# Performance work log

Hardware: AMD Instinct MI355X
Metric: run time of the kernel (lower is better)

## Reference

```python
import jax, jax.numpy as jnp
import numpy as np
import math

N, T, D, H = 64, 512, 256, 256

def setup_inputs() -> dict:
    key = jax.random.key(0)
    k1, k2, k3, k4 = jax.random.split(key, 4)
    x = jax.random.normal(k1, (N, T, D), dtype=jnp.float32)
    h0 = jax.random.normal(k2, (N, H), dtype=jnp.float32)
    Wx = jax.random.normal(k3, (D, H), dtype=jnp.float32) / math.sqrt(D)
    Wh = jax.random.normal(k4, (H, H), dtype=jnp.float32) / math.sqrt(H)
    b = jnp.zeros((H,), dtype=jnp.float32)
    return {"x": x, "h0": h0, "Wx": Wx, "Wh": Wh, "b": b}

def reference(x, h0, Wx, Wh, b):
    # Precompute input projection for all timesteps in one big GEMM: (N,T,H)
    xW = jnp.einsum("ntd,dh->nth", x, Wx) + b
    def step(prev_h, xWt):
        next_h = jnp.tanh(xWt + prev_h @ Wh)
        return next_h, next_h
    # scan over time axis; xW transposed to (T,N,H)
    _, hs = jax.lax.scan(step, h0, jnp.swapaxes(xW, 0, 1))
    return jnp.swapaxes(hs, 0, 1)  # (N,T,H)
```

## Files before the change

### kernel.cpp

```cpp
#include <hip/hip_runtime.h>
#include <hip/hip_bf16.h>
#include <cmath>


#define KDIM  256
#define HDIM  256
#define TSTEPS 512
#define NBATCH 64
#define SCAN_BLOCKS 64
#define CH_STEPS 64
#define NCH 8
#define GEMM_BLOCKS (NCH * NBATCH)
#define SMEM_BYTES 41984

__device__ __forceinline__ unsigned pack2(float lo, float hi) {
    _Float16 fa = (_Float16)lo, fb = (_Float16)hi;
    unsigned short a, b;
    __builtin_memcpy(&a, &fa, 2);
    __builtin_memcpy(&b, &fb, 2);
    return (unsigned)a | ((unsigned)b << 16);
}

#define FMAMIX16(ACC, P0,P1,P2,P3,P4,P5,P6,P7)                                 \
    asm("v_fma_mix_f32 %0, %1, %17, %0 op_sel:[0,0,0] op_sel_hi:[0,1,0]\n\t"   \
        "v_fma_mix_f32 %0, %2, %17, %0 op_sel:[0,1,0] op_sel_hi:[0,1,0]\n\t"   \
        "v_fma_mix_f32 %0, %3, %18, %0 op_sel:[0,0,0] op_sel_hi:[0,1,0]\n\t"   \
        "v_fma_mix_f32 %0, %4, %18, %0 op_sel:[0,1,0] op_sel_hi:[0,1,0]\n\t"   \
        "v_fma_mix_f32 %0, %5, %19, %0 op_sel:[0,0,0] op_sel_hi:[0,1,0]\n\t"   \
        "v_fma_mix_f32 %0, %6, %19, %0 op_sel:[0,1,0] op_sel_hi:[0,1,0]\n\t"   \
        "v_fma_mix_f32 %0, %7, %20, %0 op_sel:[0,0,0] op_sel_hi:[0,1,0]\n\t"   \
        "v_fma_mix_f32 %0, %8, %20, %0 op_sel:[0,1,0] op_sel_hi:[0,1,0]\n\t"   \
        "v_fma_mix_f32 %0, %9, %21, %0 op_sel:[0,0,0] op_sel_hi:[0,1,0]\n\t"   \
        "v_fma_mix_f32 %0, %10, %21, %0 op_sel:[0,1,0] op_sel_hi:[0,1,0]\n\t"  \
        "v_fma_mix_f32 %0, %11, %22, %0 op_sel:[0,0,0] op_sel_hi:[0,1,0]\n\t"  \
        "v_fma_mix_f32 %0, %12, %22, %0 op_sel:[0,1,0] op_sel_hi:[0,1,0]\n\t"  \
        "v_fma_mix_f32 %0, %13, %23, %0 op_sel:[0,0,0] op_sel_hi:[0,1,0]\n\t"  \
        "v_fma_mix_f32 %0, %14, %23, %0 op_sel:[0,1,0] op_sel_hi:[0,1,0]\n\t"  \
        "v_fma_mix_f32 %0, %15, %24, %0 op_sel:[0,0,0] op_sel_hi:[0,1,0]\n\t"  \
        "v_fma_mix_f32 %0, %16, %24, %0 op_sel:[0,1,0] op_sel_hi:[0,1,0]\n\t"  \
        : "+v"(ACC)                                                            \
        : "v"(h0), "v"(h1), "v"(h2), "v"(h3),                                  \
          "v"(h4), "v"(h5), "v"(h6), "v"(h7),                                  \
          "v"(h8), "v"(h9), "v"(h10), "v"(h11),                                \
          "v"(h12), "v"(h13), "v"(h14), "v"(h15),                              \
          "v"(P0), "v"(P1), "v"(P2), "v"(P3),                                  \
          "v"(P4), "v"(P5), "v"(P6), "v"(P7))

#define LDW2(K)                                                                \
    float4 ta##K = *(const float4*)(wp + (2*(K)) * HDIM);                      \
    float4 tb##K = *(const float4*)(wp + (2*(K)+1) * HDIM);                    \
    unsigned wA##K = pack2(ta##K.x, tb##K.x);                                  \
    unsigned wB##K = pack2(ta##K.y, tb##K.y);                                  \
    unsigned wC##K = pack2(ta##K.z, tb##K.z);                                  \
    unsigned wD##K = pack2(ta##K.w, tb##K.w);

#define PIN8(P)                                                                \
    asm volatile("" : "+v"(P##0), "+v"(P##1), "+v"(P##2), "+v"(P##3),          \
                      "+v"(P##4), "+v"(P##5), "+v"(P##6), "+v"(P##7))

__global__ __launch_bounds__(1024) void fused(
    const float* __restrict__ x,
    const float* __restrict__ h0v,
    const float* __restrict__ Wx,
    const float* __restrict__ Wh,
    const float* __restrict__ bias,
    float* __restrict__ out,
    unsigned int* flags,
    int mode)
{
    __shared__ __align__(16) char smem[SMEM_BYTES];
    const int tid = threadIdx.x;

    if (mode == 1 && blockIdx.x < SCAN_BLOCKS) return;
    const bool is_scan = (mode == 2) || (mode == 0 && blockIdx.x < SCAN_BLOCKS);

    if (!is_scan) {
        float (*As)[68]  = (float(*)[68])smem;
        float (*Bs)[260] = (float(*)[260])(smem + 8704);

        const int bm = (int)blockIdx.x - SCAN_BLOCKS;
        const int r  = bm & 63;
        const int ch = bm >> 6;
        const int m0 = r * TSTEPS + ch * CH_STEPS;
        const int tx = tid & 63;
        const int ty = tid >> 6;

        float acc[4][4];
#pragma unroll
        for (int i = 0; i < 4; ++i)
#pragma unroll
            for (int j = 0; j < 4; ++j) acc[i][j] = 0.f;

        for (int kc = 0; kc < KDIM; kc += 32) {
            if (tid < 512) {
                int arow = tid >> 3;
                int ac4  = (tid & 7) << 2;
                float4 va = *(const float4*)&x[(size_t)(m0 + arow) * KDIM + kc + ac4];
                As[ac4 + 0][arow] = va.x;
                As[ac4 + 1][arow] = va.y;
                As[ac4 + 2][arow] = va.z;
                As[ac4 + 3][arow] = va.w;
            }
            {
                int brow = tid >> 6;
                int bc4  = (tid & 63) << 2;
                *(float4*)&Bs[brow][bc4] =
                    *(const float4*)&Wx[(size_t)(kc + brow) * HDIM + bc4];
                *(float4*)&Bs[brow + 16][bc4] =
                    *(const float4*)&Wx[(size_t)(kc + brow + 16) * HDIM + bc4];
            }
            __syncthreads();

#pragma unroll
            for (int kk = 0; kk < 32; ++kk) {
                float4 a = *(const float4*)&As[kk][ty * 4];
                float4 b = *(const float4*)&Bs[kk][tx * 4];
                acc[0][0] += a.x * b.x; acc[0][1] += a.x * b.y;
                acc[0][2] += a.x * b.z; acc[0][3] += a.x * b.w;
                acc[1][0] += a.y * b.x; acc[1][1] += a.y * b.y;
                acc[1][2] += a.y * b.z; acc[1][3] += a.y * b.w;
                acc[2][0] += a.z * b.x; acc[2][1] += a.z * b.y;
                acc[2][2] += a.z * b.z; acc[2][3] += a.z * b.w;
                acc[3][0] += a.w * b.x; acc[3][1] += a.w * b.y;
                acc[3][2] += a.w * b.z; acc[3][3] += a.w * b.w;
            }
            __syncthreads();
        }

        float4 bj = *(const float4*)&bias[tx * 4];
#pragma unroll
        for (int i = 0; i < 4; ++i) {
            float4 v;
            v.x = acc[i][0] + bj.x;
            v.y = acc[i][1] + bj.y;
            v.z = acc[i][2] + bj.z;
            v.w = acc[i][3] + bj.w;
            *(float4*)&out[(size_t)(m0 + ty * 4 + i) * HDIM + tx * 4] = v;
        }

        if (mode == 0) {
            __syncthreads();
            if (tid == 0)
                __hip_atomic_fetch_add(&flags[r * NCH + ch], 1u,
                                       __ATOMIC_RELEASE, __HIP_MEMORY_SCOPE_AGENT);
        }
        return;
    }

    float* h = (float*)smem;
    float (*red)[256] = (float(*)[256])(smem + 1024);

    const int r   = (int)blockIdx.x;
    const int jq  = tid & 63;
    const int g   = tid >> 6;
    const int j0  = jq << 2;

    const float* wp = Wh + (size_t)(g * 16) * HDIM + j0;
    LDW2(0) LDW2(1) LDW2(2) LDW2(3) LDW2(4) LDW2(5) LDW2(6) LDW2(7)
    PIN8(wA); PIN8(wB); PIN8(wC); PIN8(wD);

    if (tid < 256) h[tid] = h0v[(size_t)r * HDIM + tid];

    float* outr = out + (size_t)r * TSTEPS * HDIM;
    __syncthreads();

    float c_next = 0.f;
    for (int ch = 0; ch < NCH; ++ch) {
        if (mode == 0) {
            if (tid == 0) {
                const unsigned int* f = &flags[r * NCH + ch];
                while (__hip_atomic_load(f, __ATOMIC_RELAXED,
                                         __HIP_MEMORY_SCOPE_AGENT) == 0u)
                    __builtin_amdgcn_s_sleep(8);
                (void)__hip_atomic_load(f, __ATOMIC_ACQUIRE,
                                        __HIP_MEMORY_SCOPE_AGENT);
            }
            __syncthreads();
        }
        if (g < 4) c_next = outr[(size_t)(ch * CH_STEPS) * HDIM + tid];

        for (int tt = 0; tt < CH_STEPS; ++tt) {
            const int t = ch * CH_STEPS + tt;
            float c = c_next;
            if (g < 4 && tt + 1 < CH_STEPS)
                c_next = outr[(size_t)(t + 1) * HDIM + tid];

            const float4* hv = (const float4*)(h + (g << 4));
            float4 ha = hv[0], hb = hv[1], hc = hv[2], hd = hv[3];
            float h0 = ha.x, h1 = ha.y, h2 = ha.z, h3 = ha.w;
            float h4 = hb.x, h5 = hb.y, h6 = hb.z, h7 = hb.w;
            float h8 = hc.x, h9 = hc.y, h10 = hc.z, h11 = hc.w;
            float h12 = hd.x, h13 = hd.y, h14 = hd.z, h15 = hd.w;

            float a0 = 0.f, a1 = 0.f, a2 = 0.f, a3 = 0.f;
            FMAMIX16(a0, wA0,wA1,wA2,wA3,wA4,wA5,wA6,wA7);
            FMAMIX16(a1, wB0,wB1,wB2,wB3,wB4,wB5,wB6,wB7);
            FMAMIX16(a2, wC0,wC1,wC2,wC3,wC4,wC5,wC6,wC7);
            FMAMIX16(a3, wD0,wD1,wD2,wD3,wD4,wD5,wD6,wD7);

            float4 accv; accv.x = a0; accv.y = a1; accv.z = a2; accv.w = a3;
            *(float4*)&red[g][j0] = accv;
            __syncthreads();

            if (tid < 256) {
                float s0 = red[0][tid] + red[1][tid];
                float s1 = red[2][tid] + red[3][tid];
                float s2 = red[4][tid] + red[5][tid];
                float s3 = red[6][tid] + red[7][tid];
                float s4 = red[8][tid] + red[9][tid];
                float s5 = red[10][tid] + red[11][tid];
                float s6 = red[12][tid] + red[13][tid];
                float s7 = red[14][tid] + red[15][tid];
                float s  = (((s0 + s1) + (s2 + s3)) + ((s4 + s5) + (s6 + s7))) + c;
                float e  = __expf(2.f * s);
                float hn = 1.f - 2.f / (e + 1.f);
                outr[(size_t)t * HDIM + tid] = hn;
                h[tid] = hn;
            }
            __syncthreads();
        }
    }
}

extern "C" void kernel_launch(void* const* d_in, const int* in_sizes, int n_in,
                              void* d_out, int out_size, void* d_ws, size_t ws_size,
                              hipStream_t stream) {
    const float* x  = (const float*)d_in[0];
    const float* h0 = (const float*)d_in[1];
    const float* Wx = (const float*)d_in[2];
    const float* Wh = (const float*)d_in[3];
    const float* b  = (const float*)d_in[4];
    float* out = (float*)d_out;

    const size_t flag_bytes = (size_t)NBATCH * NCH * sizeof(unsigned int);
    if (d_ws != nullptr && ws_size >= flag_bytes) {
        unsigned int* flags = (unsigned int*)d_ws;
        hipMemsetAsync(d_ws, 0, flag_bytes, stream);
        fused<<<SCAN_BLOCKS + GEMM_BLOCKS, 1024, 0, stream>>>(
            x, h0, Wx, Wh, b, out, flags, 0);
    } else {
        fused<<<SCAN_BLOCKS + GEMM_BLOCKS, 1024, 0, stream>>>(
            x, h0, Wx, Wh, b, out, nullptr, 1);
        fused<<<SCAN_BLOCKS, 1024, 0, stream>>>(
            x, h0, Wx, Wh, b, out, nullptr, 2);
    }
}
```

Baseline: 534.3 us.

## Prepack Wh to fp16 globally and reload weights each step to free VGPRs

Adds a small pre-kernel that packs Wh into fp16 pairs in a global buffer laid out for the scan threads. The scan loop no longer keeps the 32 packed weight registers pinned. It reloads them from the (cache-resident) packed buffer every timestep, placed after the FMAs, with an opaque index so the loads are not hoisted. This cuts register pressure and setup conversion, at the cost of an extra launch and per-step global/L2 loads on the serial critical path.

```diff
diff --git a/kernel.cpp b/kernel.cpp
--- a/kernel.cpp
+++ b/kernel.cpp
@@ -13,12 +13,29 @@
 #define GEMM_BLOCKS (NCH * NBATCH)
 #define SMEM_BYTES 41984
 
+__device__ uint4 g_Wp[8192];
+
 __device__ __forceinline__ unsigned pack2(float lo, float hi) {
     _Float16 fa = (_Float16)lo, fb = (_Float16)hi;
     unsigned short a, b;
     __builtin_memcpy(&a, &fa, 2);
     __builtin_memcpy(&b, &fb, 2);
     return (unsigned)a | ((unsigned)b << 16);
+}
+
+__global__ __launch_bounds__(256) void pack_wh(const float* __restrict__ Wh) {
+    int idx = blockIdx.x * 256 + threadIdx.x;
+    int jq = idx & 63;
+    int gp = idx >> 6;
+    int g = gp >> 3, p = gp & 7;
+    const float* r0 = Wh + (size_t)(g * 16 + 2 * p) * HDIM + jq * 4;
+    const float* r1 = r0 + HDIM;
+    uint4 o;
+    o.x = pack2(r0[0], r1[0]);
+    o.y = pack2(r0[1], r1[1]);
+    o.z = pack2(r0[2], r1[2]);
+    o.w = pack2(r0[3], r1[3]);
+    g_Wp[idx] = o;
 }
 
 #define FMAMIX16(ACC, P0,P1,P2,P3,P4,P5,P6,P7)                                 \
@@ -46,23 +63,18 @@
           "v"(P0), "v"(P1), "v"(P2), "v"(P3),                                  \
           "v"(P4), "v"(P5), "v"(P6), "v"(P7))
 
-#define LDW2(K)                                                                \
-    float4 ta##K = *(const float4*)(wp + (2*(K)) * HDIM);                      \
-    float4 tb##K = *(const float4*)(wp + (2*(K)+1) * HDIM);                    \
-    unsigned wA##K = pack2(ta##K.x, tb##K.x);                                  \
-    unsigned wB##K = pack2(ta##K.y, tb##K.y);                                  \
-    unsigned wC##K = pack2(ta##K.z, tb##K.z);                                  \
-    unsigned wD##K = pack2(ta##K.w, tb##K.w);
-
-#define PIN8(P)                                                                \
-    asm volatile("" : "+v"(P##0), "+v"(P##1), "+v"(P##2), "+v"(P##3),          \
-                      "+v"(P##4), "+v"(P##5), "+v"(P##6), "+v"(P##7))
+#define LOADW do {                                                             \
+        unsigned _i = 0;                                                       \
+        asm volatile("" : "+v"(_i));                                           \
+        const uint4* wq = wbase + _i;                                          \
+        u0 = wq[0];   u1 = wq[64];  u2 = wq[128]; u3 = wq[192];                \
+        u4 = wq[256]; u5 = wq[320]; u6 = wq[384]; u7 = wq[448];                \
+    } while (0)
 
 __global__ __launch_bounds__(1024) void fused(
     const float* __restrict__ x,
     const float* __restrict__ h0v,
     const float* __restrict__ Wx,
-    const float* __restrict__ Wh,
     const float* __restrict__ bias,
     float* __restrict__ out,
     unsigned int* flags,
@@ -155,9 +167,9 @@
     const int g   = tid >> 6;
     const int j0  = jq << 2;
 
-    const float* wp = Wh + (size_t)(g * 16) * HDIM + j0;
-    LDW2(0) LDW2(1) LDW2(2) LDW2(3) LDW2(4) LDW2(5) LDW2(6) LDW2(7)
-    PIN8(wA); PIN8(wB); PIN8(wC); PIN8(wD);
+    const uint4* wbase = g_Wp + (size_t)(g * 8) * 64 + jq;
+    uint4 u0, u1, u2, u3, u4, u5, u6, u7;
+    LOADW;
 
     if (tid < 256) h[tid] = h0v[(size_t)r * HDIM + tid];
 
@@ -193,10 +205,12 @@
             float h12 = hd.x, h13 = hd.y, h14 = hd.z, h15 = hd.w;
 
             float a0 = 0.f, a1 = 0.f, a2 = 0.f, a3 = 0.f;
-            FMAMIX16(a0, wA0,wA1,wA2,wA3,wA4,wA5,wA6,wA7);
-            FMAMIX16(a1, wB0,wB1,wB2,wB3,wB4,wB5,wB6,wB7);
-            FMAMIX16(a2, wC0,wC1,wC2,wC3,wC4,wC5,wC6,wC7);
-            FMAMIX16(a3, wD0,wD1,wD2,wD3,wD4,wD5,wD6,wD7);
+            FMAMIX16(a0, u0.x, u1.x, u2.x, u3.x, u4.x, u5.x, u6.x, u7.x);
+            FMAMIX16(a1, u0.y, u1.y, u2.y, u3.y, u4.y, u5.y, u6.y, u7.y);
+            FMAMIX16(a2, u0.z, u1.z, u2.z, u3.z, u4.z, u5.z, u6.z, u7.z);
+            FMAMIX16(a3, u0.w, u1.w, u2.w, u3.w, u4.w, u5.w, u6.w, u7.w);
+
+            LOADW;
 
             float4 accv; accv.x = a0; accv.y = a1; accv.z = a2; accv.w = a3;
             *(float4*)&red[g][j0] = accv;
@@ -232,16 +246,18 @@
     const float* b  = (const float*)d_in[4];
     float* out = (float*)d_out;
 
+    pack_wh<<<32, 256, 0, stream>>>(Wh);
+
     const size_t flag_bytes = (size_t)NBATCH * NCH * sizeof(unsigned int);
     if (d_ws != nullptr && ws_size >= flag_bytes) {
         unsigned int* flags = (unsigned int*)d_ws;
         hipMemsetAsync(d_ws, 0, flag_bytes, stream);
         fused<<<SCAN_BLOCKS + GEMM_BLOCKS, 1024, 0, stream>>>(
-            x, h0, Wx, Wh, b, out, flags, 0);
+            x, h0, Wx, b, out, flags, 0);
     } else {
         fused<<<SCAN_BLOCKS + GEMM_BLOCKS, 1024, 0, stream>>>(
-            x, h0, Wx, Wh, b, out, nullptr, 1);
+            x, h0, Wx, b, out, nullptr, 1);
         fused<<<SCAN_BLOCKS, 1024, 0, stream>>>(
-            x, h0, Wx, Wh, b, out, nullptr, 2);
+            x, h0, Wx, b, out, nullptr, 2);
     }
 }
```

Result: slower. 795.3 us (+48.9%).
